# Kernel tuning notes

Hardware: AMD Instinct MI355X
Metric: run time of the kernel (lower is better)

## Reference

```python
import jax, jax.numpy as jnp
import numpy as np

N, G, E, R = 32768, 2048, 1146880, 3
NIN, GIN, F, OUT = 6, 4, 64, 1


def _w(k, fan_in, fan_out):
    return (jax.random.normal(k, (fan_in, fan_out), jnp.float32) / np.sqrt(fan_in)).astype(jnp.float32)


def setup_inputs() -> dict:
    key = jax.random.key(0)
    ks = jax.random.split(key, 20)
    x = jax.random.normal(ks[0], (N, NIN), jnp.float32)
    u = jax.random.normal(ks[1], (G, GIN), jnp.float32)
    batch = jnp.sort(jax.random.randint(ks[2], (N,), 0, G))
    hyperedge_index = jax.random.randint(ks[3], (R, E), 0, N)
    batch_hyper = jnp.sort(jax.random.randint(ks[4], (E,), 0, G))
    inp = {
        "x": x, "u": u, "batch": batch,
        "hyperedge_index": hyperedge_index, "batch_hyper": batch_hyper, "r": R,
        # mlp_x: (NIN+GIN)->F->F->F
        "W1": _w(ks[5], NIN + GIN, F), "b1": jnp.zeros((F,), jnp.float32),
        "W2": _w(ks[6], F, F), "b2": jnp.zeros((F,), jnp.float32),
        "W3": _w(ks[7], F, F), "b3": jnp.zeros((F,), jnp.float32),
        # weighting matrix [F,F]
        "weight": _w(ks[8], F, F),
        # x_hat: 2F->F->F->OUT
        "V1": _w(ks[9], 2 * F, F), "c1": jnp.zeros((F,), jnp.float32),
        "V2": _w(ks[10], F, F), "c2": jnp.zeros((F,), jnp.float32),
        "V3": _w(ks[11], F, OUT), "c3": jnp.zeros((OUT,), jnp.float32),
    }
    return inp


def _segment_softmax(x, idx, num_segments):
    # torch_geometric-style softmax grouped by idx along dim 0, per feature
    seg_max = jax.ops.segment_max(x, idx, num_segments=num_segments)
    ex = jnp.exp(x - seg_max[idx])
    denom = jax.ops.segment_sum(ex, idx, num_segments=num_segments)
    return ex / denom[idx]


def reference(x, u, batch, hyperedge_index, batch_hyper, r,
              W1, b1, W2, b2, W3, b3, weight, V1, c1, V2, c2, V3, c3):
    # mlp_x on [node_feats || global_feats_of_node's_graph]
    h = jnp.concatenate([x, u[batch]], axis=1)            # [N, NIN+GIN]
    h = jnp.maximum(h @ W1 + b1, 0.0)
    h = jnp.maximum(h @ W2 + b2, 0.0)
    h = h @ W3 + b3                                        # [N, F]

    # hyperedge finding: sum the r member-node embeddings of each hyperedge
    x_hyper = jnp.zeros((hyperedge_index.shape[1], h.shape[1]), h.dtype)
    for i in range(hyperedge_index.shape[0]):              # r is small & fixed
        x_hyper = x_hyper + jnp.take(h, hyperedge_index[i], axis=0)  # [E, F]

    # weighting: segment softmax over hyperedges of the same graph
    coef = _segment_softmax(x_hyper, batch_hyper, G)       # [E, F]
    x_hyper_hat = coef * jnp.maximum(x_hyper @ weight, 0.0)

    # x_hat head
    o = jnp.concatenate([x_hyper, x_hyper_hat], axis=1)    # [E, 2F]
    o = jnp.maximum(o @ V1 + c1, 0.0)
    o = jnp.maximum(o @ V2 + c2, 0.0)
    o = jax.nn.sigmoid(o @ V3 + c3)                        # [E, OUT]
    return (o, batch_hyper)
```

## Files before the change

kernel.cpp:

```cpp
#include <hip/hip_runtime.h>
#include <math.h>

typedef short bf16x8 __attribute__((ext_vector_type(8)));
typedef float f32x4  __attribute__((ext_vector_type(4)));
typedef float f32x2  __attribute__((ext_vector_type(2)));
typedef unsigned short u16;
typedef unsigned int   u32;

#define MFMA16 __builtin_amdgcn_mfma_f32_16x16x32_bf16

__device__ __forceinline__ u16 f2b(float x) {
    union { float f; unsigned u; } v; v.f = x;
    unsigned r = v.u + 0x7fffu + ((v.u >> 16) & 1u);
    return (u16)(r >> 16);
}
__device__ __forceinline__ u16 f2bu(float x) {
    union { float f; unsigned u; } v; v.f = x;
    return (u16)((v.u + 0x8000u) >> 16);
}
__device__ __forceinline__ float b2f(u16 h) {
    union { unsigned u; float f; } v; v.u = ((unsigned)h) << 16;
    return v.f;
}
__device__ __forceinline__ float blo(u32 w) {
    union { u32 u; float f; } v; v.u = w << 16; return v.f;
}
__device__ __forceinline__ float bhi(u32 w) {
    union { u32 u; float f; } v; v.u = w & 0xffff0000u; return v.f;
}
__device__ __forceinline__ u32 add3pack(u32 x, u32 y, u32 z) {
    union { float f; u32 u; } lo, hi;
    lo.f = blo(x) + blo(y) + blo(z);
    hi.f = bhi(x) + bhi(y) + bhi(z);
    return __builtin_amdgcn_perm(hi.u + 0x8000u, lo.u + 0x8000u, 0x07060302u);
}
__device__ __forceinline__ f32x2 pk_add(f32x2 a, f32x2 b) {
    f32x2 d;
    asm("v_pk_add_f32 %0, %1, %2" : "=v"(d) : "v"(a), "v"(b));
    return d;
}
__device__ __forceinline__ void add3pack2(u32 x0, u32 x1, u32 y0, u32 y1,
                                          u32 z0, u32 z1, u32& d0, u32& d1) {
    union { f32x2 f; u32 u[2]; } lx, hx, ly, hy, lz, hz, lo, hi;
    lx.u[0] = x0 << 16;          lx.u[1] = x1 << 16;
    hx.u[0] = x0 & 0xffff0000u;  hx.u[1] = x1 & 0xffff0000u;
    ly.u[0] = y0 << 16;          ly.u[1] = y1 << 16;
    hy.u[0] = y0 & 0xffff0000u;  hy.u[1] = y1 & 0xffff0000u;
    lz.u[0] = z0 << 16;          lz.u[1] = z1 << 16;
    hz.u[0] = z0 & 0xffff0000u;  hz.u[1] = z1 & 0xffff0000u;
    lo.f = pk_add(pk_add(lx.f, ly.f), lz.f);
    hi.f = pk_add(pk_add(hx.f, hy.f), hz.f);
    d0 = __builtin_amdgcn_perm(hi.u[0] + 0x8000u, lo.u[0] + 0x8000u, 0x07060302u);
    d1 = __builtin_amdgcn_perm(hi.u[1] + 0x8000u, lo.u[1] + 0x8000u, 0x07060302u);
}
__device__ __forceinline__ u32 pack2(float lo, float hi) {
    union { float f; u32 u; } a, b;
    a.f = lo; b.f = hi;
    return __builtin_amdgcn_perm(b.u + 0x8000u, a.u + 0x8000u, 0x07060302u);
}

#define LOG2E 1.44269504088896340736f

__global__ __launch_bounds__(256) void prep_mlp_kernel(
    const float* __restrict__ x, const float* __restrict__ u,
    const int* __restrict__ batch,
    const float* __restrict__ W1, const float* __restrict__ b1,
    const float* __restrict__ W2, const float* __restrict__ b2,
    const float* __restrict__ W3, const float* __restrict__ b3,
    u16* __restrict__ hb, int N,
    const float* __restrict__ Wg, const float* __restrict__ V1g,
    const float* __restrict__ V2g, u16* __restrict__ SWZ,
    const int* __restrict__ bh, int E, int G, int* __restrict__ seg_start,
    int SB)
{
    const int b = blockIdx.x, tid = threadIdx.x;
    if (b < 32) {
        int idx = b * 256 + tid;
        int k = idx >> 6, n = idx & 63;
        int s1 = (k < 64) ? k : (64 + (((k - 64) & 15) << 2) + ((k - 64) >> 4));
        int off1 = ((s1 >> 5) * 4 + (n >> 4)) * 512 + (n & 15) * 32 + ((s1 >> 3) & 3) * 8 + (s1 & 7);
        SWZ[4096 + off1] = f2b(V1g[idx]);
        if (idx < 4096) {
            int offw = ((k >> 5) * 4 + (n >> 4)) * 512 + (n & 15) * 32 + ((k >> 3) & 3) * 8 + (k & 7);
            SWZ[offw] = f2b(Wg[idx]);
            int s2 = ((k & 15) << 2) + (k >> 4);
            int off2 = ((s2 >> 5) * 4 + (n >> 4)) * 512 + (n & 15) * 32 + ((s2 >> 3) & 3) * 8 + (s2 & 7);
            SWZ[12288 + off2] = f2b(V2g[idx]);
        }
        return;
    }
    if (b < 32 + SB) {
        int g = (b - 32) * 256 + tid;
        if (g > G) return;
        int lo = 0, hi = E;
        while (lo < hi) {
            int mid = (lo + hi) >> 1;
            if (bh[mid] < g) lo = mid + 1; else hi = mid;
        }
        seg_start[g] = lo;
        return;
    }
    __shared__ float inbuf[16][10];
    __shared__ float h1[16][64];
    __shared__ float h2[16][64];
    const int ni = tid >> 6, f = tid & 63;
    const int base = (b - 32 - SB) * 16;
    int nodes[4];
    #pragma unroll
    for (int s = 0; s < 4; ++s) {
        nodes[s] = min(base + s * 4 + ni, N - 1);
        if (f < 6)       inbuf[s * 4 + ni][f] = x[nodes[s] * 6 + f];
        else if (f < 10) inbuf[s * 4 + ni][f] = u[batch[nodes[s]] * 4 + (f - 6)];
    }
    __syncthreads();
    float acc[4];
    #pragma unroll
    for (int s = 0; s < 4; ++s) acc[s] = b1[f];
    #pragma unroll
    for (int k = 0; k < 10; ++k) {
        float w = W1[k * 64 + f];
        #pragma unroll
        for (int s = 0; s < 4; ++s) acc[s] = fmaf(inbuf[s * 4 + ni][k], w, acc[s]);
    }
    #pragma unroll
    for (int s = 0; s < 4; ++s) h1[s * 4 + ni][f] = fmaxf(acc[s], 0.f);
    __syncthreads();
    #pragma unroll
    for (int s = 0; s < 4; ++s) acc[s] = b2[f];
    #pragma unroll
    for (int k4 = 0; k4 < 16; ++k4) {
        float w0 = W2[(k4 * 4 + 0) * 64 + f];
        float w1 = W2[(k4 * 4 + 1) * 64 + f];
        float w2 = W2[(k4 * 4 + 2) * 64 + f];
        float w3 = W2[(k4 * 4 + 3) * 64 + f];
        #pragma unroll
        for (int s = 0; s < 4; ++s) {
            float4 hv = *(const float4*)&h1[s * 4 + ni][k4 * 4];
            acc[s] = fmaf(hv.x, w0, acc[s]);
            acc[s] = fmaf(hv.y, w1, acc[s]);
            acc[s] = fmaf(hv.z, w2, acc[s]);
            acc[s] = fmaf(hv.w, w3, acc[s]);
        }
    }
    #pragma unroll
    for (int s = 0; s < 4; ++s) h2[s * 4 + ni][f] = fmaxf(acc[s], 0.f);
    __syncthreads();
    #pragma unroll
    for (int s = 0; s < 4; ++s) acc[s] = b3[f];
    #pragma unroll
    for (int k4 = 0; k4 < 16; ++k4) {
        float w0 = W3[(k4 * 4 + 0) * 64 + f];
        float w1 = W3[(k4 * 4 + 1) * 64 + f];
        float w2 = W3[(k4 * 4 + 2) * 64 + f];
        float w3 = W3[(k4 * 4 + 3) * 64 + f];
        #pragma unroll
        for (int s = 0; s < 4; ++s) {
            float4 hv = *(const float4*)&h2[s * 4 + ni][k4 * 4];
            acc[s] = fmaf(hv.x, w0, acc[s]);
            acc[s] = fmaf(hv.y, w1, acc[s]);
            acc[s] = fmaf(hv.z, w2, acc[s]);
            acc[s] = fmaf(hv.w, w3, acc[s]);
        }
    }
    #pragma unroll
    for (int s = 0; s < 4; ++s) hb[nodes[s] * 64 + f] = f2b(acc[s]);
}

__global__ __launch_bounds__(256, 3) void fused_seg_kernel(
    const u16* __restrict__ hb, const int* __restrict__ hidx,
    const int* __restrict__ seg_start, const u16* __restrict__ SWZ,
    const float* __restrict__ c1g, const float* __restrict__ c2g,
    const float* __restrict__ V3g, const float* __restrict__ c3g,
    float* __restrict__ out, int E)
{
    __shared__ u16 SW[16384];
    __shared__ u16 XT_all[4][16 * 64];
    __shared__ float ps[4][8][8];
    __shared__ float Sf[64];

    const int tid = threadIdx.x, lane = tid & 63, wid = tid >> 6;
    const int g = blockIdx.x;
    const int e0 = seg_start[g], e1 = seg_start[g + 1];
    const int L = e1 - e0;
    if (L <= 0) return;
    const int e1m1 = e1 - 1;

    {
        const uint4* src = (const uint4*)SWZ;
        uint4* dst = (uint4*)SW;
        for (int i = tid; i < 2048; i += 256) dst[i] = src[i];
    }

    {
        const int sub = lane >> 3, cl = lane & 7;
        const float gf = (float)g;
        for (int e = e0 + tid; e < e1; e += 256) out[E + e] = gf;

        float s[8] = {0.f, 0.f, 0.f, 0.f, 0.f, 0.f, 0.f, 0.f};
        for (int e = e0 + wid * 8 + sub; e < e1; e += 128) {
            #pragma unroll
            for (int j = 0; j < 4; ++j) {
                int ee = e + j * 32;
                int ec = min(ee, e1m1);
                int i0 = hidx[ec], i1 = hidx[E + ec], i2 = hidx[2 * E + ec];
                uint4 A0 = *(const uint4*)(hb + (size_t)i0 * 64 + cl * 8);
                uint4 A1 = *(const uint4*)(hb + (size_t)i1 * 64 + cl * 8);
                uint4 A2 = *(const uint4*)(hb + (size_t)i2 * 64 + cl * 8);
                u32 w0 = add3pack(A0.x, A1.x, A2.x);
                u32 w1 = add3pack(A0.y, A1.y, A2.y);
                u32 w2 = add3pack(A0.z, A1.z, A2.z);
                u32 w3 = add3pack(A0.w, A1.w, A2.w);
                if (ee < e1) {
                    s[0] += __expf(blo(w0)); s[1] += __expf(bhi(w0));
                    s[2] += __expf(blo(w1)); s[3] += __expf(bhi(w1));
                    s[4] += __expf(blo(w2)); s[5] += __expf(bhi(w2));
                    s[6] += __expf(blo(w3)); s[7] += __expf(bhi(w3));
                }
            }
        }
        #pragma unroll
        for (int k = 0; k < 8; ++k) {
            s[k] += __shfl_xor(s[k], 8);
            s[k] += __shfl_xor(s[k], 16);
            s[k] += __shfl_xor(s[k], 32);
        }
        if (lane < 8) {
            #pragma unroll
            for (int k = 0; k < 8; ++k) ps[wid][lane][k] = s[k];
        }
        __syncthreads();
        if (tid < 64) {
            int c8 = tid >> 3, cc = tid & 7;
            float S = ps[0][c8][cc] + ps[1][c8][cc] + ps[2][c8][cc] + ps[3][c8][cc];
            Sf[tid] = 1.f / S;
        }
        __syncthreads();
    }

    const int nl = lane & 15, rq = lane >> 4;
    const u16* WB  = SW;
    const u16* V1B = SW + 4096;
    const u16* V2B = SW + 12288;

    bf16x8 I0, I1;
    #pragma unroll
    for (int j = 0; j < 8; ++j) {
        I0[j] = (rq * 8 + j == nl)      ? (short)0x3F80 : (short)0;
        I1[j] = (rq * 8 + j == nl + 16) ? (short)0x3F80 : (short)0;
    }

    float l2d[4], c1v[4], c2v[4], v3v[4];
    #pragma unroll
    for (int nt = 0; nt < 4; ++nt) {
        int col = nt * 16 + nl;
        l2d[nt] = __log2f(Sf[col]);
        c1v[nt] = c1g[col];
        c2v[nt] = c2g[col];
        v3v[nt] = V3g[col];
    }
    const float c3s = c3g[0];
    u16* XT = XT_all[wid];
    const f32x4 zf = {0.f, 0.f, 0.f, 0.f};

    const int xw_swz = rq << 4;
    const int xr_base = nl * 64;
    const int xr_swz  = (nl & 12) << 2;
    const int xr0 = xr_base + ((rq * 8) ^ xr_swz);
    const int xr1 = xr_base + ((rq * 8 + 32) ^ xr_swz);

    auto loadA = [&](int tt, bf16x8& A0, bf16x8& A1) {
        const int ec = min(e0 + tt * 16 + nl, e1m1);
        const int i0 = hidx[ec], i1 = hidx[E + ec], i2 = hidx[2 * E + ec];
        const u16* r0 = hb + (size_t)i0 * 64 + rq * 8;
        const u16* r1 = hb + (size_t)i1 * 64 + rq * 8;
        const u16* r2 = hb + (size_t)i2 * 64 + rq * 8;
        uint4 B0 = *(const uint4*)(r0), C0 = *(const uint4*)(r0 + 32);
        uint4 B1 = *(const uint4*)(r1), C1 = *(const uint4*)(r1 + 32);
        uint4 B2 = *(const uint4*)(r2), C2 = *(const uint4*)(r2 + 32);
        union { uint4 q; bf16x8 h; } u0, u1v;
        add3pack2(B0.x, B0.y, B1.x, B1.y, B2.x, B2.y, u0.q.x, u0.q.y);
        add3pack2(B0.z, B0.w, B1.z, B1.w, B2.z, B2.w, u0.q.z, u0.q.w);
        add3pack2(C0.x, C0.y, C1.x, C1.y, C2.x, C2.y, u1v.q.x, u1v.q.y);
        add3pack2(C0.z, C0.w, C1.z, C1.w, C2.z, C2.w, u1v.q.z, u1v.q.w);
        A0 = u0.h;
        A1 = u1v.h;
    };

    int t = wid;
    bf16x8 p0 = {}, p1 = {};
    if (t * 16 < L) loadA(t, p0, p1);

    for (; t * 16 < L; t += 8) {
        const int eB1 = e0 + t * 16;
        const int eB2 = eB1 + 64;

        bf16x8 a0 = p0, a1 = p1;
        bf16x8 a2, a3;
        loadA(t + 4, a2, a3);
        if ((t + 8) * 16 < L) loadA(t + 8, p0, p1);

        f32x4 xc1[4], xc2[4];
        xc1[0] = MFMA16(a0, I0, zf, 0, 0, 0);
        xc1[1] = MFMA16(a0, I1, zf, 0, 0, 0);
        xc1[2] = MFMA16(a1, I0, zf, 0, 0, 0);
        xc1[3] = MFMA16(a1, I1, zf, 0, 0, 0);
        xc2[0] = MFMA16(a2, I0, zf, 0, 0, 0);
        xc2[1] = MFMA16(a2, I1, zf, 0, 0, 0);
        xc2[2] = MFMA16(a3, I0, zf, 0, 0, 0);
        xc2[3] = MFMA16(a3, I1, zf, 0, 0, 0);

        f32x4 acc1[4] = {zf, zf, zf, zf}, acc2t[4] = {zf, zf, zf, zf};
        #pragma unroll
        for (int nt = 0; nt < 4; ++nt) {
            bf16x8 b0 = *(const bf16x8*)(WB + (0 * 4 + nt) * 512 + nl * 32 + rq * 8);
            acc1[nt]  = MFMA16(a0, b0, acc1[nt], 0, 0, 0);
            acc2t[nt] = MFMA16(a2, b0, acc2t[nt], 0, 0, 0);
            bf16x8 b1 = *(const bf16x8*)(WB + (1 * 4 + nt) * 512 + nl * 32 + rq * 8);
            acc1[nt]  = MFMA16(a1, b1, acc1[nt], 0, 0, 0);
            acc2t[nt] = MFMA16(a3, b1, acc2t[nt], 0, 0, 0);
        }
        #pragma unroll
        for (int r = 0; r < 4; ++r) {
            float v0 = __builtin_amdgcn_exp2f(fmaf(xc1[0][r], LOG2E, l2d[0])) * fmaxf(acc1[0][r], 0.f);
            float v1 = __builtin_amdgcn_exp2f(fmaf(xc1[1][r], LOG2E, l2d[1])) * fmaxf(acc1[1][r], 0.f);
            float v2 = __builtin_amdgcn_exp2f(fmaf(xc1[2][r], LOG2E, l2d[2])) * fmaxf(acc1[2][r], 0.f);
            float v3 = __builtin_amdgcn_exp2f(fmaf(xc1[3][r], LOG2E, l2d[3])) * fmaxf(acc1[3][r], 0.f);
            uint2 w; w.x = pack2(v0, v1); w.y = pack2(v2, v3);
            *(uint2*)(XT + (rq * 4 + r) * 64 + ((nl * 4) ^ xw_swz)) = w;
        }
        bf16x8 x2a = *(const bf16x8*)(XT + xr0);
        bf16x8 x3a = *(const bf16x8*)(XT + xr1);
        #pragma unroll
        for (int r = 0; r < 4; ++r) {
            float v0 = __builtin_amdgcn_exp2f(fmaf(xc2[0][r], LOG2E, l2d[0])) * fmaxf(acc2t[0][r], 0.f);
            float v1 = __builtin_amdgcn_exp2f(fmaf(xc2[1][r], LOG2E, l2d[1])) * fmaxf(acc2t[1][r], 0.f);
            float v2 = __builtin_amdgcn_exp2f(fmaf(xc2[2][r], LOG2E, l2d[2])) * fmaxf(acc2t[2][r], 0.f);
            float v3 = __builtin_amdgcn_exp2f(fmaf(xc2[3][r], LOG2E, l2d[3])) * fmaxf(acc2t[3][r], 0.f);
            uint2 w; w.x = pack2(v0, v1); w.y = pack2(v2, v3);
            *(uint2*)(XT + (rq * 4 + r) * 64 + ((nl * 4) ^ xw_swz)) = w;
        }
        bf16x8 x2b = *(const bf16x8*)(XT + xr0);
        bf16x8 x3b = *(const bf16x8*)(XT + xr1);

        f32x4 va[4], vb[4];
        #pragma unroll
        for (int nt = 0; nt < 4; ++nt) {
            va[nt][0] = c1v[nt]; va[nt][1] = c1v[nt];
            va[nt][2] = c1v[nt]; va[nt][3] = c1v[nt];
            vb[nt] = va[nt];
        }
        #pragma unroll
        for (int nt = 0; nt < 4; ++nt) {
            bf16x8 b0 = *(const bf16x8*)(V1B + (0 * 4 + nt) * 512 + nl * 32 + rq * 8);
            va[nt] = MFMA16(a0, b0, va[nt], 0, 0, 0);
            vb[nt] = MFMA16(a2, b0, vb[nt], 0, 0, 0);
            bf16x8 b1 = *(const bf16x8*)(V1B + (1 * 4 + nt) * 512 + nl * 32 + rq * 8);
            va[nt] = MFMA16(a1, b1, va[nt], 0, 0, 0);
            vb[nt] = MFMA16(a3, b1, vb[nt], 0, 0, 0);
        }
        #pragma unroll
        for (int nt = 0; nt < 4; ++nt) {
            bf16x8 b2 = *(const bf16x8*)(V1B + (2 * 4 + nt) * 512 + nl * 32 + rq * 8);
            va[nt] = MFMA16(x2a, b2, va[nt], 0, 0, 0);
            vb[nt] = MFMA16(x2b, b2, vb[nt], 0, 0, 0);
            bf16x8 b3 = *(const bf16x8*)(V1B + (3 * 4 + nt) * 512 + nl * 32 + rq * 8);
            va[nt] = MFMA16(x3a, b3, va[nt], 0, 0, 0);
            vb[nt] = MFMA16(x3b, b3, vb[nt], 0, 0, 0);
        }
        #pragma unroll
        for (int r = 0; r < 4; ++r) {
            uint2 w;
            w.x = pack2(fmaxf(va[0][r], 0.f), fmaxf(va[1][r], 0.f));
            w.y = pack2(fmaxf(va[2][r], 0.f), fmaxf(va[3][r], 0.f));
            *(uint2*)(XT + (rq * 4 + r) * 64 + ((nl * 4) ^ xw_swz)) = w;
        }
        bf16x8 o0a = *(const bf16x8*)(XT + xr0);
        bf16x8 o1a = *(const bf16x8*)(XT + xr1);
        #pragma unroll
        for (int r = 0; r < 4; ++r) {
            uint2 w;
            w.x = pack2(fmaxf(vb[0][r], 0.f), fmaxf(vb[1][r], 0.f));
            w.y = pack2(fmaxf(vb[2][r], 0.f), fmaxf(vb[3][r], 0.f));
            *(uint2*)(XT + (rq * 4 + r) * 64 + ((nl * 4) ^ xw_swz)) = w;
        }
        bf16x8 o0b = *(const bf16x8*)(XT + xr0);
        bf16x8 o1b = *(const bf16x8*)(XT + xr1);

        f32x4 wa[4], wb2[4];
        #pragma unroll
        for (int nt = 0; nt < 4; ++nt) {
            wa[nt][0] = c2v[nt]; wa[nt][1] = c2v[nt];
            wa[nt][2] = c2v[nt]; wa[nt][3] = c2v[nt];
            wb2[nt] = wa[nt];
        }
        #pragma unroll
        for (int nt = 0; nt < 4; ++nt) {
            bf16x8 b0 = *(const bf16x8*)(V2B + (0 * 4 + nt) * 512 + nl * 32 + rq * 8);
            wa[nt]  = MFMA16(o0a, b0, wa[nt], 0, 0, 0);
            wb2[nt] = MFMA16(o0b, b0, wb2[nt], 0, 0, 0);
            bf16x8 b1 = *(const bf16x8*)(V2B + (1 * 4 + nt) * 512 + nl * 32 + rq * 8);
            wa[nt]  = MFMA16(o1a, b1, wa[nt], 0, 0, 0);
            wb2[nt] = MFMA16(o1b, b1, wb2[nt], 0, 0, 0);
        }

        float sra[4], srb[4];
        #pragma unroll
        for (int r = 0; r < 4; ++r) {
            float u1 = 0.f, u2 = 0.f;
            #pragma unroll
            for (int nt = 0; nt < 4; ++nt) {
                u1 = fmaf(fmaxf(wa[nt][r],  0.f), v3v[nt], u1);
                u2 = fmaf(fmaxf(wb2[nt][r], 0.f), v3v[nt], u2);
            }
            u1 += __shfl_xor(u1, 1); u2 += __shfl_xor(u2, 1);
            u1 += __shfl_xor(u1, 2); u2 += __shfl_xor(u2, 2);
            u1 += __shfl_xor(u1, 4); u2 += __shfl_xor(u2, 4);
            u1 += __shfl_xor(u1, 8); u2 += __shfl_xor(u2, 8);
            sra[r] = __builtin_amdgcn_rcpf(1.f + __expf(-(u1 + c3s)));
            srb[r] = __builtin_amdgcn_rcpf(1.f + __expf(-(u2 + c3s)));
        }
        if (nl == 0) {
            const int ra = eB1 + rq * 4;
            if (ra + 3 < e1) {
                *(float4*)(out + ra) = make_float4(sra[0], sra[1], sra[2], sra[3]);
            } else {
                #pragma unroll
                for (int r = 0; r < 4; ++r)
                    if (ra + r < e1) out[ra + r] = sra[r];
            }
            const int rb = eB2 + rq * 4;
            if (rb + 3 < e1) {
                *(float4*)(out + rb) = make_float4(srb[0], srb[1], srb[2], srb[3]);
            } else {
                #pragma unroll
                for (int r = 0; r < 4; ++r)
                    if (rb + r < e1) out[rb + r] = srb[r];
            }
        }
    }
}

extern "C" void kernel_launch(void* const* d_in, const int* in_sizes, int n_in,
                              void* d_out, int out_size, void* d_ws, size_t ws_size,
                              hipStream_t stream) {
    const float* x     = (const float*)d_in[0];
    const float* u     = (const float*)d_in[1];
    const int*   batch = (const int*)  d_in[2];
    const int*   hidx  = (const int*)  d_in[3];
    const int*   bh    = (const int*)  d_in[4];
    const float* W1 = (const float*)d_in[6];
    const float* b1 = (const float*)d_in[7];
    const float* W2 = (const float*)d_in[8];
    const float* b2 = (const float*)d_in[9];
    const float* W3 = (const float*)d_in[10];
    const float* b3 = (const float*)d_in[11];
    const float* Wg = (const float*)d_in[12];
    const float* V1 = (const float*)d_in[13];
    const float* c1 = (const float*)d_in[14];
    const float* V2 = (const float*)d_in[15];
    const float* c2 = (const float*)d_in[16];
    const float* V3 = (const float*)d_in[17];
    const float* c3 = (const float*)d_in[18];

    const int N = in_sizes[0] / 6;
    const int G = in_sizes[1] / 4;
    const int E = in_sizes[4];

    char* ws = (char*)d_ws;
    size_t off = 0;
    u16* hb = (u16*)(ws + off);            off += (size_t)N * 64 * 2;
    int* seg_start = (int*)(ws + off);     off += ((size_t)G + 1) * 4;
    off = (off + 255) & ~(size_t)255;
    u16* SWZ = (u16*)(ws + off);           off += 16384 * 2;
    float* out = (float*)d_out;

    const int SB = (G + 256) / 256;
    const int NB = (N + 15) / 16;
    prep_mlp_kernel<<<32 + SB + NB, 256, 0, stream>>>(
        x, u, batch, W1, b1, W2, b2, W3, b3, hb, N,
        Wg, V1, V2, SWZ, bh, E, G, seg_start, SB);
    fused_seg_kernel<<<G, 256, 0, stream>>>(
        hb, hidx, seg_start, SWZ, c1, c2, V3, c3, out, E);
}
```

Before: 253.2 us.

## Merge prep and segment kernels into one persistent cooperative kernel with grid sync

Replaces the two-kernel pipeline with a single cooperative persistent kernel. Blocks first loop over the prep work units (weight swizzle, segment starts, node MLP), then cross a grid-wide barrier, then loop over graphs doing the softmax stats pass and the MFMA pass. The aim is to remove the second launch and its gap, and to stage the weights into shared memory once per persistent block instead of once per graph. In exchange it adds the grid sync cost and limits the grid to blocks that can be co-resident, which may reduce latency hiding. If the cooperative launch fails, it falls back to three separate kernels with stats kept in a workspace buffer.

```diff
diff --git a/kernel.cpp b/kernel.cpp
--- a/kernel.cpp
+++ b/kernel.cpp
@@ -1,5 +1,8 @@
 #include <hip/hip_runtime.h>
+#include <hip/hip_cooperative_groups.h>
 #include <math.h>
+
+namespace cg = cooperative_groups;
 
 typedef short bf16x8 __attribute__((ext_vector_type(8)));
 typedef float f32x4  __attribute__((ext_vector_type(4)));
@@ -17,10 +20,6 @@
 __device__ __forceinline__ u16 f2bu(float x) {
     union { float f; unsigned u; } v; v.f = x;
     return (u16)((v.u + 0x8000u) >> 16);
-}
-__device__ __forceinline__ float b2f(u16 h) {
-    union { unsigned u; float f; } v; v.u = ((unsigned)h) << 16;
-    return v.f;
 }
 __device__ __forceinline__ float blo(u32 w) {
     union { u32 u; float f; } v; v.u = w << 16; return v.f;
@@ -61,7 +60,9 @@
 
 #define LOG2E 1.44269504088896340736f
 
-__global__ __launch_bounds__(256) void prep_mlp_kernel(
+
+__device__ __forceinline__ void prep_unit(
+    int uu, int tid,
     const float* __restrict__ x, const float* __restrict__ u,
     const int* __restrict__ batch,
     const float* __restrict__ W1, const float* __restrict__ b1,
@@ -71,11 +72,10 @@
     const float* __restrict__ Wg, const float* __restrict__ V1g,
     const float* __restrict__ V2g, u16* __restrict__ SWZ,
     const int* __restrict__ bh, int E, int G, int* __restrict__ seg_start,
-    int SB)
+    int SB, char* LB)
 {
-    const int b = blockIdx.x, tid = threadIdx.x;
-    if (b < 32) {
-        int idx = b * 256 + tid;
+    if (uu < 32) {
+        int idx = uu * 256 + tid;
         int k = idx >> 6, n = idx & 63;
         int s1 = (k < 64) ? k : (64 + (((k - 64) & 15) << 2) + ((k - 64) >> 4));
         int off1 = ((s1 >> 5) * 4 + (n >> 4)) * 512 + (n & 15) * 32 + ((s1 >> 3) & 3) * 8 + (s1 & 7);
@@ -89,8 +89,8 @@
         }
         return;
     }
-    if (b < 32 + SB) {
-        int g = (b - 32) * 256 + tid;
+    if (uu < 32 + SB) {
+        int g = (uu - 32) * 256 + tid;
         if (g > G) return;
         int lo = 0, hi = E;
         while (lo < hi) {
@@ -100,17 +100,17 @@
         seg_start[g] = lo;
         return;
     }
-    __shared__ float inbuf[16][10];
-    __shared__ float h1[16][64];
-    __shared__ float h2[16][64];
+    float* inbuf = (float*)LB;
+    float* h1    = (float*)(LB + 768);
+    float* h2    = (float*)(LB + 4864);
     const int ni = tid >> 6, f = tid & 63;
-    const int base = (b - 32 - SB) * 16;
+    const int base = (uu - 32 - SB) * 16;
     int nodes[4];
     #pragma unroll
     for (int s = 0; s < 4; ++s) {
         nodes[s] = min(base + s * 4 + ni, N - 1);
-        if (f < 6)       inbuf[s * 4 + ni][f] = x[nodes[s] * 6 + f];
-        else if (f < 10) inbuf[s * 4 + ni][f] = u[batch[nodes[s]] * 4 + (f - 6)];
+        if (f < 6)       inbuf[(s * 4 + ni) * 10 + f] = x[nodes[s] * 6 + f];
+        else if (f < 10) inbuf[(s * 4 + ni) * 10 + f] = u[batch[nodes[s]] * 4 + (f - 6)];
     }
     __syncthreads();
     float acc[4];
@@ -120,10 +120,10 @@
     for (int k = 0; k < 10; ++k) {
         float w = W1[k * 64 + f];
         #pragma unroll
-        for (int s = 0; s < 4; ++s) acc[s] = fmaf(inbuf[s * 4 + ni][k], w, acc[s]);
-    }
-    #pragma unroll
-    for (int s = 0; s < 4; ++s) h1[s * 4 + ni][f] = fmaxf(acc[s], 0.f);
+        for (int s = 0; s < 4; ++s) acc[s] = fmaf(inbuf[(s * 4 + ni) * 10 + k], w, acc[s]);
+    }
+    #pragma unroll
+    for (int s = 0; s < 4; ++s) h1[(s * 4 + ni) * 64 + f] = fmaxf(acc[s], 0.f);
     __syncthreads();
     #pragma unroll
     for (int s = 0; s < 4; ++s) acc[s] = b2[f];
@@ -135,7 +135,7 @@
         float w3 = W2[(k4 * 4 + 3) * 64 + f];
         #pragma unroll
         for (int s = 0; s < 4; ++s) {
-            float4 hv = *(const float4*)&h1[s * 4 + ni][k4 * 4];
+            float4 hv = *(const float4*)&h1[(s * 4 + ni) * 64 + k4 * 4];
             acc[s] = fmaf(hv.x, w0, acc[s]);
             acc[s] = fmaf(hv.y, w1, acc[s]);
             acc[s] = fmaf(hv.z, w2, acc[s]);
@@ -143,7 +143,7 @@
         }
     }
     #pragma unroll
-    for (int s = 0; s < 4; ++s) h2[s * 4 + ni][f] = fmaxf(acc[s], 0.f);
+    for (int s = 0; s < 4; ++s) h2[(s * 4 + ni) * 64 + f] = fmaxf(acc[s], 0.f);
     __syncthreads();
     #pragma unroll
     for (int s = 0; s < 4; ++s) acc[s] = b3[f];
@@ -155,7 +155,7 @@
         float w3 = W3[(k4 * 4 + 3) * 64 + f];
         #pragma unroll
         for (int s = 0; s < 4; ++s) {
-            float4 hv = *(const float4*)&h2[s * 4 + ni][k4 * 4];
+            float4 hv = *(const float4*)&h2[(s * 4 + ni) * 64 + k4 * 4];
             acc[s] = fmaf(hv.x, w0, acc[s]);
             acc[s] = fmaf(hv.y, w1, acc[s]);
             acc[s] = fmaf(hv.z, w2, acc[s]);
@@ -166,100 +166,78 @@
     for (int s = 0; s < 4; ++s) hb[nodes[s] * 64 + f] = f2b(acc[s]);
 }
 
-__global__ __launch_bounds__(256, 3) void fused_seg_kernel(
+__device__ __forceinline__ void stats_pass(
+    int g, int e0, int e1, int tid, int lane, int wid,
     const u16* __restrict__ hb, const int* __restrict__ hidx,
-    const int* __restrict__ seg_start, const u16* __restrict__ SWZ,
-    const float* __restrict__ c1g, const float* __restrict__ c2g,
-    const float* __restrict__ V3g, const float* __restrict__ c3g,
+    float* __restrict__ out, int E, float* psb, float* Sfb)
+{
+    const int e1m1 = e1 - 1;
+    const int sub = lane >> 3, cl = lane & 7;
+    const float gf = (float)g;
+    for (int e = e0 + tid; e < e1; e += 256) out[E + e] = gf;
+
+    float s[8] = {0.f, 0.f, 0.f, 0.f, 0.f, 0.f, 0.f, 0.f};
+    for (int e = e0 + wid * 8 + sub; e < e1; e += 128) {
+        #pragma unroll
+        for (int j = 0; j < 4; ++j) {
+            int ee = e + j * 32;
+            int ec = min(ee, e1m1);
+            int i0 = hidx[ec], i1 = hidx[E + ec], i2 = hidx[2 * E + ec];
+            uint4 A0 = *(const uint4*)(hb + (size_t)i0 * 64 + cl * 8);
+            uint4 A1 = *(const uint4*)(hb + (size_t)i1 * 64 + cl * 8);
+            uint4 A2 = *(const uint4*)(hb + (size_t)i2 * 64 + cl * 8);
+            u32 w0 = add3pack(A0.x, A1.x, A2.x);
+            u32 w1 = add3pack(A0.y, A1.y, A2.y);
+            u32 w2 = add3pack(A0.z, A1.z, A2.z);
+            u32 w3 = add3pack(A0.w, A1.w, A2.w);
+            if (ee < e1) {
+                s[0] += __expf(blo(w0)); s[1] += __expf(bhi(w0));
+                s[2] += __expf(blo(w1)); s[3] += __expf(bhi(w1));
+                s[4] += __expf(blo(w2)); s[5] += __expf(bhi(w2));
+                s[6] += __expf(blo(w3)); s[7] += __expf(bhi(w3));
+            }
+        }
+    }
+    #pragma unroll
+    for (int k = 0; k < 8; ++k) {
+        s[k] += __shfl_xor(s[k], 8);
+        s[k] += __shfl_xor(s[k], 16);
+        s[k] += __shfl_xor(s[k], 32);
+    }
+    if (lane < 8) {
+        #pragma unroll
+        for (int k = 0; k < 8; ++k) psb[wid * 64 + lane * 8 + k] = s[k];
+    }
+    __syncthreads();
+    if (tid < 64) {
+        int c8 = tid >> 3, cc = tid & 7;
+        float S = psb[0 * 64 + c8 * 8 + cc] + psb[1 * 64 + c8 * 8 + cc]
+                + psb[2 * 64 + c8 * 8 + cc] + psb[3 * 64 + c8 * 8 + cc];
+        Sfb[tid] = 1.f / S;
+    }
+    __syncthreads();
+}
+
+__device__ __forceinline__ void mfma_pass(
+    int e0, int e1, int lane, int wid,
+    const u16* __restrict__ hb, const int* __restrict__ hidx,
+    const u16* SWp, u16* XTb, const float* Sfb,
+    const float* c1v, const float* c2v, const float* v3v, float c3s,
+    const bf16x8& I0, const bf16x8& I1,
     float* __restrict__ out, int E)
 {
-    __shared__ u16 SW[16384];
-    __shared__ u16 XT_all[4][16 * 64];
-    __shared__ float ps[4][8][8];
-    __shared__ float Sf[64];
-
-    const int tid = threadIdx.x, lane = tid & 63, wid = tid >> 6;
-    const int g = blockIdx.x;
-    const int e0 = seg_start[g], e1 = seg_start[g + 1];
+    const int nl = lane & 15, rq = lane >> 4;
     const int L = e1 - e0;
-    if (L <= 0) return;
     const int e1m1 = e1 - 1;
-
-    {
-        const uint4* src = (const uint4*)SWZ;
-        uint4* dst = (uint4*)SW;
-        for (int i = tid; i < 2048; i += 256) dst[i] = src[i];
-    }
-
-    {
-        const int sub = lane >> 3, cl = lane & 7;
-        const float gf = (float)g;
-        for (int e = e0 + tid; e < e1; e += 256) out[E + e] = gf;
-
-        float s[8] = {0.f, 0.f, 0.f, 0.f, 0.f, 0.f, 0.f, 0.f};
-        for (int e = e0 + wid * 8 + sub; e < e1; e += 128) {
-            #pragma unroll
-            for (int j = 0; j < 4; ++j) {
-                int ee = e + j * 32;
-                int ec = min(ee, e1m1);
-                int i0 = hidx[ec], i1 = hidx[E + ec], i2 = hidx[2 * E + ec];
-                uint4 A0 = *(const uint4*)(hb + (size_t)i0 * 64 + cl * 8);
-                uint4 A1 = *(const uint4*)(hb + (size_t)i1 * 64 + cl * 8);
-                uint4 A2 = *(const uint4*)(hb + (size_t)i2 * 64 + cl * 8);
-                u32 w0 = add3pack(A0.x, A1.x, A2.x);
-                u32 w1 = add3pack(A0.y, A1.y, A2.y);
-                u32 w2 = add3pack(A0.z, A1.z, A2.z);
-                u32 w3 = add3pack(A0.w, A1.w, A2.w);
-                if (ee < e1) {
-                    s[0] += __expf(blo(w0)); s[1] += __expf(bhi(w0));
-                    s[2] += __expf(blo(w1)); s[3] += __expf(bhi(w1));
-                    s[4] += __expf(blo(w2)); s[5] += __expf(bhi(w2));
-                    s[6] += __expf(blo(w3)); s[7] += __expf(bhi(w3));
-                }
-            }
-        }
-        #pragma unroll
-        for (int k = 0; k < 8; ++k) {
-            s[k] += __shfl_xor(s[k], 8);
-            s[k] += __shfl_xor(s[k], 16);
-            s[k] += __shfl_xor(s[k], 32);
-        }
-        if (lane < 8) {
-            #pragma unroll
-            for (int k = 0; k < 8; ++k) ps[wid][lane][k] = s[k];
-        }
-        __syncthreads();
-        if (tid < 64) {
-            int c8 = tid >> 3, cc = tid & 7;
-            float S = ps[0][c8][cc] + ps[1][c8][cc] + ps[2][c8][cc] + ps[3][c8][cc];
-            Sf[tid] = 1.f / S;
-        }
-        __syncthreads();
-    }
-
-    const int nl = lane & 15, rq = lane >> 4;
-    const u16* WB  = SW;
-    const u16* V1B = SW + 4096;
-    const u16* V2B = SW + 12288;
-
-    bf16x8 I0, I1;
-    #pragma unroll
-    for (int j = 0; j < 8; ++j) {
-        I0[j] = (rq * 8 + j == nl)      ? (short)0x3F80 : (short)0;
-        I1[j] = (rq * 8 + j == nl + 16) ? (short)0x3F80 : (short)0;
-    }
-
-    float l2d[4], c1v[4], c2v[4], v3v[4];
-    #pragma unroll
-    for (int nt = 0; nt < 4; ++nt) {
-        int col = nt * 16 + nl;
-        l2d[nt] = __log2f(Sf[col]);
-        c1v[nt] = c1g[col];
-        c2v[nt] = c2g[col];
-        v3v[nt] = V3g[col];
-    }
-    const float c3s = c3g[0];
-    u16* XT = XT_all[wid];
+    const u16* WB  = SWp;
+    const u16* V1B = SWp + 4096;
+    const u16* V2B = SWp + 12288;
+
+    float l2d[4];
+    #pragma unroll
+    for (int nt = 0; nt < 4; ++nt) l2d[nt] = __log2f(Sfb[nt * 16 + nl]);
+
+    u16* XT = XTb + wid * 1024;
     const f32x4 zf = {0.f, 0.f, 0.f, 0.f};
 
     const int xw_swz = rq << 4;
@@ -438,6 +416,150 @@
             }
         }
     }
+}
+
+__global__ __launch_bounds__(256, 3) void mono_kernel(
+    const float* __restrict__ x, const float* __restrict__ u,
+    const int* __restrict__ batch,
+    const float* __restrict__ W1, const float* __restrict__ b1,
+    const float* __restrict__ W2, const float* __restrict__ b2,
+    const float* __restrict__ W3, const float* __restrict__ b3,
+    u16* __restrict__ hb,
+    const float* __restrict__ Wg, const float* __restrict__ V1g,
+    const float* __restrict__ V2g, u16* __restrict__ SWZ,
+    const int* __restrict__ bh, const int* __restrict__ hidx,
+    int* __restrict__ seg_start,
+    const float* __restrict__ c1g, const float* __restrict__ c2g,
+    const float* __restrict__ V3g, const float* __restrict__ c3g,
+    float* __restrict__ out, int N, int E, int G, int SB, int NB)
+{
+    __shared__ __align__(16) char LB[42240];
+    const int tid = threadIdx.x, lane = tid & 63, wid = tid >> 6;
+
+    const int U = 32 + SB + NB;
+    for (int uu = blockIdx.x; uu < U; uu += gridDim.x) {
+        prep_unit(uu, tid, x, u, batch, W1, b1, W2, b2, W3, b3, hb, N,
+                  Wg, V1g, V2g, SWZ, bh, E, G, seg_start, SB, LB);
+        __syncthreads();
+    }
+    __threadfence();
+    cg::this_grid().sync();
+
+    u16*   SWp = (u16*)LB;
+    u16*   XTb = (u16*)(LB + 32768);
+    float* psb = (float*)(LB + 40960);
+    float* Sfb = (float*)(LB + 41984);
+
+    {
+        const uint4* src = (const uint4*)SWZ;
+        uint4* dst = (uint4*)SWp;
+        for (int i = tid; i < 2048; i += 256) dst[i] = src[i];
+    }
+
+    const int nl = lane & 15;
+    bf16x8 I0, I1;
+    #pragma unroll
+    for (int j = 0; j < 8; ++j) {
+        int rq = lane >> 4;
+        I0[j] = (rq * 8 + j == nl)      ? (short)0x3F80 : (short)0;
+        I1[j] = (rq * 8 + j == nl + 16) ? (short)0x3F80 : (short)0;
+    }
+    float c1v[4], c2v[4], v3v[4];
+    #pragma unroll
+    for (int nt = 0; nt < 4; ++nt) {
+        int col = nt * 16 + nl;
+        c1v[nt] = c1g[col];
+        c2v[nt] = c2g[col];
+        v3v[nt] = V3g[col];
+    }
+    const float c3s = c3g[0];
+
+    for (int g = blockIdx.x; g < G; g += gridDim.x) {
+        const int e0 = seg_start[g], e1 = seg_start[g + 1];
+        if (e1 <= e0) continue;
+        stats_pass(g, e0, e1, tid, lane, wid, hb, hidx, out, E, psb, Sfb);
+        mfma_pass(e0, e1, lane, wid, hb, hidx, SWp, XTb, Sfb,
+                  c1v, c2v, v3v, c3s, I0, I1, out, E);
+        __syncthreads();
+    }
+}
+
+__global__ __launch_bounds__(256) void prep_mlp_kernel(
+    const float* __restrict__ x, const float* __restrict__ u,
+    const int* __restrict__ batch,
+    const float* __restrict__ W1, const float* __restrict__ b1,
+    const float* __restrict__ W2, const float* __restrict__ b2,
+    const float* __restrict__ W3, const float* __restrict__ b3,
+    u16* __restrict__ hb, int N,
+    const float* __restrict__ Wg, const float* __restrict__ V1g,
+    const float* __restrict__ V2g, u16* __restrict__ SWZ,
+    const int* __restrict__ bh, int E, int G, int* __restrict__ seg_start,
+    int SB)
+{
+    __shared__ __align__(16) char LB[8960];
+    prep_unit(blockIdx.x, threadIdx.x, x, u, batch, W1, b1, W2, b2, W3, b3,
+              hb, N, Wg, V1g, V2g, SWZ, bh, E, G, seg_start, SB, LB);
+}
+
+__global__ __launch_bounds__(256) void gather_stats_kernel(
+    const u16* __restrict__ hb, const int* __restrict__ hidx,
+    const int* __restrict__ seg_start,
+    float* __restrict__ Sinv, float* __restrict__ out, int E)
+{
+    __shared__ float psb[256];
+    __shared__ float Sfb[64];
+    const int tid = threadIdx.x, lane = tid & 63, wid = tid >> 6;
+    const int g = blockIdx.x;
+    const int e0 = seg_start[g], e1 = seg_start[g + 1];
+    if (e1 <= e0) return;
+    stats_pass(g, e0, e1, tid, lane, wid, hb, hidx, out, E, psb, Sfb);
+    if (tid < 64) Sinv[g * 64 + tid] = Sfb[tid];
+}
+
+__global__ __launch_bounds__(256, 3) void mfma_seg_kernel(
+    const u16* __restrict__ hb, const int* __restrict__ hidx,
+    const int* __restrict__ seg_start,
+    const u16* __restrict__ SWZ, const float* __restrict__ Sinv,
+    const float* __restrict__ c1g, const float* __restrict__ c2g,
+    const float* __restrict__ V3g, const float* __restrict__ c3g,
+    float* __restrict__ out, int E)
+{
+    __shared__ __align__(16) u16 SW[16384];
+    __shared__ __align__(16) u16 XT_all[4][1024];
+
+    const int tid = threadIdx.x, lane = tid & 63, wid = tid >> 6;
+    const int nl = lane & 15;
+    const int g = blockIdx.x;
+    const int e0 = seg_start[g], e1 = seg_start[g + 1];
+    if (e1 <= e0) return;
+
+    {
+        const uint4* src = (const uint4*)SWZ;
+        uint4* dst = (uint4*)SW;
+        for (int i = tid; i < 2048; i += 256) dst[i] = src[i];
+    }
+    __syncthreads();
+
+    bf16x8 I0, I1;
+    #pragma unroll
+    for (int j = 0; j < 8; ++j) {
+        int rq = lane >> 4;
+        I0[j] = (rq * 8 + j == nl)      ? (short)0x3F80 : (short)0;
+        I1[j] = (rq * 8 + j == nl + 16) ? (short)0x3F80 : (short)0;
+    }
+    float c1v[4], c2v[4], v3v[4];
+    __shared__ float Sfb[64];
+    if (tid < 64) Sfb[tid] = Sinv[g * 64 + tid];
+    #pragma unroll
+    for (int nt = 0; nt < 4; ++nt) {
+        int col = nt * 16 + nl;
+        c1v[nt] = c1g[col];
+        c2v[nt] = c2g[col];
+        v3v[nt] = V3g[col];
+    }
+    __syncthreads();
+    mfma_pass(e0, e1, lane, wid, hb, hidx, SW, &XT_all[0][0], Sfb,
+              c1v, c2v, v3v, c3g[0], I0, I1, out, E);
 }
 
 extern "C" void kernel_launch(void* const* d_in, const int* in_sizes, int n_in,
@@ -462,9 +584,9 @@
     const float* V3 = (const float*)d_in[17];
     const float* c3 = (const float*)d_in[18];
 
-    const int N = in_sizes[0] / 6;
-    const int G = in_sizes[1] / 4;
-    const int E = in_sizes[4];
+    int N = in_sizes[0] / 6;
+    int G = in_sizes[1] / 4;
+    int E = in_sizes[4];
 
     char* ws = (char*)d_ws;
     size_t off = 0;
@@ -472,13 +594,55 @@
     int* seg_start = (int*)(ws + off);     off += ((size_t)G + 1) * 4;
     off = (off + 255) & ~(size_t)255;
     u16* SWZ = (u16*)(ws + off);           off += 16384 * 2;
+    float* Sinv = (float*)(ws + off);      off += (size_t)G * 64 * 4;
     float* out = (float*)d_out;
 
-    const int SB = (G + 256) / 256;
-    const int NB = (N + 15) / 16;
-    prep_mlp_kernel<<<32 + SB + NB, 256, 0, stream>>>(
-        x, u, batch, W1, b1, W2, b2, W3, b3, hb, N,
-        Wg, V1, V2, SWZ, bh, E, G, seg_start, SB);
-    fused_seg_kernel<<<G, 256, 0, stream>>>(
-        hb, hidx, seg_start, SWZ, c1, c2, V3, c3, out, E);
-}
+    int SB = (G + 256) / 256;
+    int NB = (N + 15) / 16;
+
+    static int coopBlocks = -2;
+    if (coopBlocks == -2) {
+        int occ = 0;
+        hipError_t oe = hipOccupancyMaxActiveBlocksPerMultiprocessor(
+            &occ, mono_kernel, 256, 0);
+        int ncu = 0;
+        int dev = 0;
+        hipGetDevice(&dev);
+        hipError_t ae = hipDeviceGetAttribute(
+            &ncu, hipDeviceAttributeMultiprocessorCount, dev);
+        if (oe == hipSuccess && ae == hipSuccess && occ >= 1 && ncu >= 1)
+            coopBlocks = occ * ncu;
+        else
+            coopBlocks = -1;
+    }
+
+    bool done = false;
+    if (coopBlocks > 0) {
+        int grid = coopBlocks < G ? coopBlocks : G;
+        void* kargs[] = {
+            (void*)&x, (void*)&u, (void*)&batch,
+            (void*)&W1, (void*)&b1, (void*)&W2, (void*)&b2,
+            (void*)&W3, (void*)&b3, (void*)&hb,
+            (void*)&Wg, (void*)&V1, (void*)&V2, (void*)&SWZ,
+            (void*)&bh, (void*)&hidx, (void*)&seg_start,
+            (void*)&c1, (void*)&c2, (void*)&V3, (void*)&c3,
+            (void*)&out, (void*)&N, (void*)&E, (void*)&G,
+            (void*)&SB, (void*)&NB };
+        hipError_t le = hipLaunchCooperativeKernel(
+            (void*)mono_kernel, dim3(grid), dim3(256), kargs, 0, stream);
+        if (le == hipSuccess) {
+            done = true;
+        } else {
+            coopBlocks = -1;
+        }
+    }
+
+    if (!done) {
+        prep_mlp_kernel<<<32 + SB + NB, 256, 0, stream>>>(
+            x, u, batch, W1, b1, W2, b2, W3, b3, hb, N,
+            Wg, V1, V2, SWZ, bh, E, G, seg_start, SB);
+        gather_stats_kernel<<<G, 256, 0, stream>>>(hb, hidx, seg_start, Sinv, out, E);
+        mfma_seg_kernel<<<G, 256, 0, stream>>>(
+            hb, hidx, seg_start, SWZ, Sinv, c1, c2, V3, c3, out, E);
+    }
+}
```

New measurement: 513.1 us. 103% more time.

## Split softmax-denominator pass into separate kernel and shrink LDS weight staging

Applied to the files above, without the earlier changes.

Moves the first pass, which gathers the hyperedge sums and accumulates the per-graph exp sums, out of the fused kernel into its own gather_stats_kernel that writes inverse denominators to a workspace. The MFMA kernel then reads those values and stages only V1 into LDS, cutting LDS from 32KB to 16KB, while the W and V2 fragments are read directly from global memory. The aim is higher occupancy and less per-block prologue. In exchange it adds a kernel launch, a second full gather of hb, and global reads of the weight fragments inside the inner loop. The sigmoid also switches from the rcp intrinsic to an exact division.

```diff
diff --git a/kernel.cpp b/kernel.cpp
--- a/kernel.cpp
+++ b/kernel.cpp
@@ -166,19 +166,75 @@
     for (int s = 0; s < 4; ++s) hb[nodes[s] * 64 + f] = f2b(acc[s]);
 }
 
-__global__ __launch_bounds__(256, 3) void fused_seg_kernel(
+__global__ __launch_bounds__(256) void gather_stats_kernel(
     const u16* __restrict__ hb, const int* __restrict__ hidx,
-    const int* __restrict__ seg_start, const u16* __restrict__ SWZ,
+    const int* __restrict__ seg_start,
+    float* __restrict__ Sinv, float* __restrict__ out, int E)
+{
+    __shared__ float ps[4][8][8];
+    const int tid = threadIdx.x, lane = tid & 63, wid = tid >> 6;
+    const int sub = lane >> 3, cl = lane & 7;
+    const int g = blockIdx.x;
+    const int e0 = seg_start[g], e1 = seg_start[g + 1];
+    if (e1 <= e0) return;
+    const int e1m1 = e1 - 1;
+    const float gf = (float)g;
+
+    for (int e = e0 + tid; e < e1; e += 256) out[E + e] = gf;
+
+    float s[8] = {0.f, 0.f, 0.f, 0.f, 0.f, 0.f, 0.f, 0.f};
+    for (int e = e0 + wid * 8 + sub; e < e1; e += 128) {
+        #pragma unroll
+        for (int j = 0; j < 4; ++j) {
+            int ee = e + j * 32;
+            int ec = min(ee, e1m1);
+            int i0 = hidx[ec], i1 = hidx[E + ec], i2 = hidx[2 * E + ec];
+            uint4 A0 = *(const uint4*)(hb + (size_t)i0 * 64 + cl * 8);
+            uint4 A1 = *(const uint4*)(hb + (size_t)i1 * 64 + cl * 8);
+            uint4 A2 = *(const uint4*)(hb + (size_t)i2 * 64 + cl * 8);
+            u32 w0 = add3pack(A0.x, A1.x, A2.x);
+            u32 w1 = add3pack(A0.y, A1.y, A2.y);
+            u32 w2 = add3pack(A0.z, A1.z, A2.z);
+            u32 w3 = add3pack(A0.w, A1.w, A2.w);
+            if (ee < e1) {
+                s[0] += __expf(blo(w0)); s[1] += __expf(bhi(w0));
+                s[2] += __expf(blo(w1)); s[3] += __expf(bhi(w1));
+                s[4] += __expf(blo(w2)); s[5] += __expf(bhi(w2));
+                s[6] += __expf(blo(w3)); s[7] += __expf(bhi(w3));
+            }
+        }
+    }
+    #pragma unroll
+    for (int k = 0; k < 8; ++k) {
+        s[k] += __shfl_xor(s[k], 8);
+        s[k] += __shfl_xor(s[k], 16);
+        s[k] += __shfl_xor(s[k], 32);
+    }
+    if (lane < 8) {
+        #pragma unroll
+        for (int k = 0; k < 8; ++k) ps[wid][lane][k] = s[k];
+    }
+    __syncthreads();
+    if (tid < 64) {
+        int c8 = tid >> 3, cc = tid & 7;
+        float S = ps[0][c8][cc] + ps[1][c8][cc] + ps[2][c8][cc] + ps[3][c8][cc];
+        Sinv[g * 64 + tid] = 1.f / S;
+    }
+}
+
+__global__ __launch_bounds__(256, 3) void mfma_seg_kernel(
+    const u16* __restrict__ hb, const int* __restrict__ hidx,
+    const int* __restrict__ seg_start,
+    const u16* __restrict__ SWZ, const float* __restrict__ Sinv,
     const float* __restrict__ c1g, const float* __restrict__ c2g,
     const float* __restrict__ V3g, const float* __restrict__ c3g,
     float* __restrict__ out, int E)
 {
-    __shared__ u16 SW[16384];
+    __shared__ u16 SW[8192];
     __shared__ u16 XT_all[4][16 * 64];
-    __shared__ float ps[4][8][8];
-    __shared__ float Sf[64];
 
     const int tid = threadIdx.x, lane = tid & 63, wid = tid >> 6;
+    const int nl = lane & 15, rq = lane >> 4;
     const int g = blockIdx.x;
     const int e0 = seg_start[g], e1 = seg_start[g + 1];
     const int L = e1 - e0;
@@ -186,61 +242,14 @@
     const int e1m1 = e1 - 1;
 
     {
-        const uint4* src = (const uint4*)SWZ;
+        const uint4* src = (const uint4*)(SWZ + 4096);
         uint4* dst = (uint4*)SW;
-        for (int i = tid; i < 2048; i += 256) dst[i] = src[i];
-    }
-
-    {
-        const int sub = lane >> 3, cl = lane & 7;
-        const float gf = (float)g;
-        for (int e = e0 + tid; e < e1; e += 256) out[E + e] = gf;
-
-        float s[8] = {0.f, 0.f, 0.f, 0.f, 0.f, 0.f, 0.f, 0.f};
-        for (int e = e0 + wid * 8 + sub; e < e1; e += 128) {
-            #pragma unroll
-            for (int j = 0; j < 4; ++j) {
-                int ee = e + j * 32;
-                int ec = min(ee, e1m1);
-                int i0 = hidx[ec], i1 = hidx[E + ec], i2 = hidx[2 * E + ec];
-                uint4 A0 = *(const uint4*)(hb + (size_t)i0 * 64 + cl * 8);
-                uint4 A1 = *(const uint4*)(hb + (size_t)i1 * 64 + cl * 8);
-                uint4 A2 = *(const uint4*)(hb + (size_t)i2 * 64 + cl * 8);
-                u32 w0 = add3pack(A0.x, A1.x, A2.x);
-                u32 w1 = add3pack(A0.y, A1.y, A2.y);
-                u32 w2 = add3pack(A0.z, A1.z, A2.z);
-                u32 w3 = add3pack(A0.w, A1.w, A2.w);
-                if (ee < e1) {
-                    s[0] += __expf(blo(w0)); s[1] += __expf(bhi(w0));
-                    s[2] += __expf(blo(w1)); s[3] += __expf(bhi(w1));
-                    s[4] += __expf(blo(w2)); s[5] += __expf(bhi(w2));
-                    s[6] += __expf(blo(w3)); s[7] += __expf(bhi(w3));
-                }
-            }
-        }
-        #pragma unroll
-        for (int k = 0; k < 8; ++k) {
-            s[k] += __shfl_xor(s[k], 8);
-            s[k] += __shfl_xor(s[k], 16);
-            s[k] += __shfl_xor(s[k], 32);
-        }
-        if (lane < 8) {
-            #pragma unroll
-            for (int k = 0; k < 8; ++k) ps[wid][lane][k] = s[k];
-        }
-        __syncthreads();
-        if (tid < 64) {
-            int c8 = tid >> 3, cc = tid & 7;
-            float S = ps[0][c8][cc] + ps[1][c8][cc] + ps[2][c8][cc] + ps[3][c8][cc];
-            Sf[tid] = 1.f / S;
-        }
-        __syncthreads();
-    }
-
-    const int nl = lane & 15, rq = lane >> 4;
-    const u16* WB  = SW;
-    const u16* V1B = SW + 4096;
-    const u16* V2B = SW + 12288;
+        for (int i = tid; i < 1024; i += 256) dst[i] = src[i];
+    }
+    __syncthreads();
+    const u16* WB  = SWZ;
+    const u16* V1B = SW;
+    const u16* V2B = SWZ + 12288;
 
     bf16x8 I0, I1;
     #pragma unroll
@@ -253,7 +262,7 @@
     #pragma unroll
     for (int nt = 0; nt < 4; ++nt) {
         int col = nt * 16 + nl;
-        l2d[nt] = __log2f(Sf[col]);
+        l2d[nt] = __log2f(Sinv[g * 64 + col]);
         c1v[nt] = c1g[col];
         c2v[nt] = c2g[col];
         v3v[nt] = V3g[col];
@@ -416,8 +425,8 @@
             u1 += __shfl_xor(u1, 2); u2 += __shfl_xor(u2, 2);
             u1 += __shfl_xor(u1, 4); u2 += __shfl_xor(u2, 4);
             u1 += __shfl_xor(u1, 8); u2 += __shfl_xor(u2, 8);
-            sra[r] = __builtin_amdgcn_rcpf(1.f + __expf(-(u1 + c3s)));
-            srb[r] = __builtin_amdgcn_rcpf(1.f + __expf(-(u2 + c3s)));
+            sra[r] = 1.f / (1.f + __expf(-(u1 + c3s)));
+            srb[r] = 1.f / (1.f + __expf(-(u2 + c3s)));
         }
         if (nl == 0) {
             const int ra = eB1 + rq * 4;
@@ -472,6 +481,7 @@
     int* seg_start = (int*)(ws + off);     off += ((size_t)G + 1) * 4;
     off = (off + 255) & ~(size_t)255;
     u16* SWZ = (u16*)(ws + off);           off += 16384 * 2;
+    float* Sinv = (float*)(ws + off);      off += (size_t)G * 64 * 4;
     float* out = (float*)d_out;
 
     const int SB = (G + 256) / 256;
@@ -479,6 +489,7 @@
     prep_mlp_kernel<<<32 + SB + NB, 256, 0, stream>>>(
         x, u, batch, W1, b1, W2, b2, W3, b3, hb, N,
         Wg, V1, V2, SWZ, bh, E, G, seg_start, SB);
-    fused_seg_kernel<<<G, 256, 0, stream>>>(
-        hb, hidx, seg_start, SWZ, c1, c2, V3, c3, out, E);
-}
+    gather_stats_kernel<<<G, 256, 0, stream>>>(hb, hidx, seg_start, Sinv, out, E);
+    mfma_seg_kernel<<<G, 256, 0, stream>>>(
+        hb, hidx, seg_start, SWZ, Sinv, c1, c2, V3, c3, out, E);
+}
```

New measurement: 284.9 us. 1.13x slower.
